# Kernel optimization log

Measured on AMD Instinct MI355X. Metric: run time of the kernel, lower is better.

The kernel has to match this reference:

```python
import jax, jax.numpy as jnp
import numpy as np

B, T, C, H = 4, 4096, 1024, 64

def setup_inputs() -> dict:
    key = jax.random.key(0)
    kx, kq, kk, kv = jax.random.split(key, 4)
    # nn.Linear weights are [out, in]; we store them that way and use einsum.
    s = 1.0 / np.sqrt(C)
    return {
        "x": jax.random.normal(kx, (B, T, C), dtype=jnp.float32),
        "Wq": jax.random.uniform(kq, (H, C), dtype=jnp.float32, minval=-s, maxval=s),
        "Wk": jax.random.uniform(kk, (H, C), dtype=jnp.float32, minval=-s, maxval=s),
        "Wv": jax.random.uniform(kv, (H, C), dtype=jnp.float32, minval=-s, maxval=s),
    }

def reference(x, Wq, Wk, Wv):
    # x: [B, T, C]; W*: [H, C] (torch Linear layout)
    Q = jnp.einsum('btc,hc->bth', x, Wq)  # [B, T, H]
    K = jnp.einsum('btc,hc->bth', x, Wk)
    V = jnp.einsum('btc,hc->bth', x, Wv)
    scale = K.shape[-1] ** -0.5
    scores = jnp.einsum('bqh,bkh->bqk', Q, K) * scale  # [B, T, T]
    Tn = x.shape[1]
    causal = jnp.tril(jnp.ones((Tn, Tn), dtype=bool))
    scores = jnp.where(causal, scores, -jnp.inf)
    attn = jax.nn.softmax(scores, axis=-1)
    return jnp.einsum('bqk,bkh->bqh', attn, V)  # [B, T, H]
```

## Files before the change

kernel.cpp:

```cpp
#include <hip/hip_runtime.h>
#include <hip/hip_bf16.h>

#define B_ 4
#define T_ 4096
#define C_ 1024
#define H_ 64

typedef __bf16 bf16x8 __attribute__((ext_vector_type(8)));
typedef float f32x4 __attribute__((ext_vector_type(4)));
typedef unsigned short u16x8 __attribute__((ext_vector_type(8)));

union Frag8 { uint4 u; bf16x8 b; u16x8 s; };

__device__ inline unsigned short bfbits(float f) {
  union { __hip_bfloat16 h; unsigned short u; } cv;
  cv.h = __float2bfloat16(f);
  return cv.u;
}

__device__ inline float b2f(unsigned u) {
  union { unsigned i; float f; } c; c.i = u << 16; return c.f;
}

__device__ inline bf16x8 ldb8(const unsigned short* p) {
  Frag8 f; f.u = *(const uint4*)p; return f.b;
}

__device__ inline bf16x8 asbf(uint4 u) { Frag8 f; f.u = u; return f.b; }

__device__ inline unsigned pkbf(float a, float b) {
  union { float f; unsigned u; } ua, ub; ua.f = a; ub.f = b;
  return __builtin_amdgcn_perm(ub.u + 0x8000u, ua.u + 0x8000u, 0x07060302u);
}

__device__ inline Frag8 packA(float4 a0, float4 a1) {
  Frag8 af;
  af.s[0] = bfbits(a0.x); af.s[1] = bfbits(a0.y);
  af.s[2] = bfbits(a0.z); af.s[3] = bfbits(a0.w);
  af.s[4] = bfbits(a1.x); af.s[5] = bfbits(a1.y);
  af.s[6] = bfbits(a1.z); af.s[7] = bfbits(a1.w);
  return af;
}

__device__ inline void gload16(const void* g, void* l) {
  __builtin_amdgcn_global_load_lds(
      (const __attribute__((address_space(1))) unsigned int*)g,
      (__attribute__((address_space(3))) unsigned int*)l, 16, 0, 0);
}

__global__ __launch_bounds__(256) void wconv(const float* __restrict__ Wq,
                                             const float* __restrict__ Wk,
                                             const float* __restrict__ Wv,
                                             unsigned short* __restrict__ Wb) {
  int i = blockIdx.x * 256 + threadIdx.x;
  size_t e = (size_t)i * 4;
  const float* src = (e < 65536) ? (Wq + e)
                   : (e < 131072 ? (Wk + (e - 65536)) : (Wv + (e - 131072)));
  float4 v = *(const float4*)src;
  unsigned long long o =
      (unsigned long long)bfbits(v.x)
    | ((unsigned long long)bfbits(v.y) << 16)
    | ((unsigned long long)bfbits(v.z) << 32)
    | ((unsigned long long)bfbits(v.w) << 48);
  *(unsigned long long*)(Wb + e) = o;
}

__global__ __launch_bounds__(256) void qkv_proj(const float* __restrict__ x,
                                                const unsigned short* __restrict__ Wb,
                                                unsigned short* __restrict__ qkv,
                                                unsigned short* __restrict__ Vt) {
  __shared__ float xs[2][2048];
  __shared__ unsigned short Wsh[2][12288];
  const int lane = threadIdx.x & 63;
  const int wave = threadIdx.x >> 6;
  const int q16 = lane & 15, quad = lane >> 4;
  const int x7 = q16 & 7;
  const size_t row0 = (size_t)blockIdx.x * 32;

  const int sr = lane >> 4;
  const int sc_pos = lane & 15;
  const int rloc = lane >> 3;
  const int cpos = lane & 7;

  f32x4 acc[2][3] = {};

  auto stage = [&](int buf, int kc) {
#pragma unroll
    for (int ii = 0; ii < 2; ++ii) {
      int i = wave * 2 + ii;
      int r = i * 4 + sr;
      int sg = (sc_pos >> 1) ^ (r & 7);
      const float* gp = x + (row0 + r) * C_ + kc + sg * 8 + (sc_pos & 1) * 4;
      gload16(gp, &xs[buf][i * 256]);
    }
#pragma unroll
    for (int jj = 0; jj < 6; ++jj) {
      int j = wave * 6 + jj;
      int g = j * 8 + rloc;
      const unsigned short* gp = Wb + (size_t)(g >> 6) * 65536
                                    + (size_t)(g & 63) * C_ + kc + (cpos ^ rloc) * 8;
      gload16(gp, &Wsh[buf][j * 512]);
    }
  };

  stage(0, 0);
  __syncthreads();

  int cur = 0;
  for (int t = 0; t < 16; ++t) {
    if (t < 15) stage(cur ^ 1, (t + 1) * 64);
    const float* Xc = xs[cur];
    const unsigned short* Wc = Wsh[cur];
#pragma unroll
    for (int s = 0; s < 2; ++s) {
      bf16x8 bf[3];
#pragma unroll
      for (int ct = 0; ct < 3; ++ct) {
        int g = wave * 48 + ct * 16 + q16;
        bf[ct] = ldb8(&Wc[g * 64 + (((s * 4 + quad) ^ x7) * 8)]);
      }
#pragma unroll
      for (int rt = 0; rt < 2; ++rt) {
        int r = rt * 16 + q16;
        int p = ((s * 4 + quad) ^ (r & 7)) * 8;
        const float* ap = &Xc[r * 64 + p];
        float4 a0 = *(const float4*)ap;
        float4 a1 = *(const float4*)(ap + 4);
        Frag8 af = packA(a0, a1);
#pragma unroll
        for (int ct = 0; ct < 3; ++ct)
          acc[rt][ct] = __builtin_amdgcn_mfma_f32_16x16x32_bf16(
              af.b, bf[ct], acc[rt][ct], 0, 0, 0);
      }
    }
    __syncthreads();
    cur ^= 1;
  }

  const int bb = (int)(blockIdx.x >> 7);
#pragma unroll
  for (int rt = 0; rt < 2; ++rt) {
    const int t0 = (int)(row0 - (size_t)bb * T_) + rt * 16 + quad * 4;
#pragma unroll
    for (int ct = 0; ct < 3; ++ct) {
      int gcol = wave * 48 + ct * 16;
      int mat = gcol >> 6, h = (gcol & 63) + q16;
      if (mat == 2) {
        ushort4 v;
        v.x = bfbits(acc[rt][ct][0]); v.y = bfbits(acc[rt][ct][1]);
        v.z = bfbits(acc[rt][ct][2]); v.w = bfbits(acc[rt][ct][3]);
        *(ushort4*)(Vt + ((size_t)bb * H_ + h) * T_ + t0) = v;
      } else {
        float scale = (mat == 0) ? 0.18033688f : 1.0f;
#pragma unroll
        for (int r = 0; r < 4; ++r) {
          size_t row = row0 + rt * 16 + quad * 4 + r;
          qkv[(size_t)mat * 1048576 + row * H_ + h] = bfbits(acc[rt][ct][r] * scale);
        }
      }
    }
  }
}

__global__ __launch_bounds__(256) void attn(const unsigned short* __restrict__ Q,
                                            const unsigned short* __restrict__ K,
                                            const unsigned short* __restrict__ Vt,
                                            float* __restrict__ part,
                                            int lgch, int nslots) {
  const int b = blockIdx.x >> 6;
  const int qblk = 63 - (blockIdx.x & 63);
  const int ki = qblk + 1;
  const int c = blockIdx.y;
  const int cst = c << lgch;
  if (cst >= ki) return;
  const int tcnt = 1 << lgch;
  const int kend = (ki < cst + tcnt) ? ki : cst + tcnt;

  __shared__ unsigned short Ks[2][4096];
  __shared__ unsigned short Vs[2][4096];
  const int lane = threadIdx.x & 63;
  const int wave = threadIdx.x >> 6;
  const int q16 = lane & 15, quad = lane >> 4;
  const int x7 = q16 & 7;
  const int rloc = lane >> 3, cpos = lane & 7;

  const unsigned short* Qb = Q + (size_t)b * T_ * H_;
  const unsigned short* Kb = K + (size_t)b * T_ * H_;
  const unsigned short* Vtb = Vt + (size_t)b * H_ * T_;

  auto stage = [&](int buf, int kt) {
    const int kkb = kt * 64;
#pragma unroll
    for (int ii = 0; ii < 2; ++ii) {
      int i = wave * 2 + ii;
      gload16(Kb + (size_t)(kkb + i * 8 + rloc) * H_ + (cpos ^ rloc) * 8,
              &Ks[buf][i * 512]);
      gload16(Vtb + (size_t)(i * 8 + rloc) * T_ + kkb + (cpos ^ rloc) * 8,
              &Vs[buf][i * 512]);
    }
  };

  const int q0w = qblk * 64 + wave * 16;
  bf16x8 qf0 = ldb8(Qb + (size_t)(q0w + q16) * H_ + quad * 8);
  bf16x8 qf1 = ldb8(Qb + (size_t)(q0w + q16) * H_ + 32 + quad * 8);

  f32x4 o0 = {0.f, 0.f, 0.f, 0.f}, o1 = o0, o2 = o0, o3 = o0;
  float m = -3.0e38f, l = 0.0f;
  const int q_abs = q0w + q16;
  const int src0 = q16 + 32 * (quad & 1);
  const int kbsel = quad >> 1;

  stage(0, cst);
  __syncthreads();

  int cur = 0;
  for (int kt = cst; kt < kend; ++kt) {
    const int kkb = kt * 64;
    if (kt + 1 < kend) stage(cur ^ 1, kt + 1);
    const unsigned short* Kc = Ks[cur];
    const unsigned short* Vc = Vs[cur];

    f32x4 st[4];
#pragma unroll
    for (int kb = 0; kb < 4; ++kb) {
      bf16x8 ka0 = ldb8(&Kc[(kb * 16 + q16) * 64 + ((quad ^ x7) * 8)]);
      bf16x8 ka1 = ldb8(&Kc[(kb * 16 + q16) * 64 + (((quad + 4) ^ x7) * 8)]);
      f32x4 s = {0.f, 0.f, 0.f, 0.f};
      s = __builtin_amdgcn_mfma_f32_16x16x32_bf16(ka0, qf0, s, 0, 0, 0);
      s = __builtin_amdgcn_mfma_f32_16x16x32_bf16(ka1, qf1, s, 0, 0, 0);
      st[kb] = s;
    }
    if (kt == ki - 1) {
#pragma unroll
      for (int kb = 0; kb < 4; ++kb)
#pragma unroll
        for (int r = 0; r < 4; ++r)
          if (kkb + kb * 16 + quad * 4 + r > q_abs) st[kb][r] = -3.0e38f;
    }

    float mloc = fmaxf(fmaxf(st[0][0], st[0][1]), fmaxf(st[0][2], st[0][3]));
#pragma unroll
    for (int kb = 1; kb < 4; ++kb)
      mloc = fmaxf(mloc, fmaxf(fmaxf(st[kb][0], st[kb][1]), fmaxf(st[kb][2], st[kb][3])));
    mloc = fmaxf(mloc, __shfl_xor(mloc, 16));
    mloc = fmaxf(mloc, __shfl_xor(mloc, 32));
    const bool defer = __all(mloc - m <= 8.0f);
    const float mnew = defer ? m : fmaxf(m, mloc);
    float lsum = 0.f;
    unsigned pk[4][2];
#pragma unroll
    for (int kb = 0; kb < 4; ++kb) {
      float p0 = exp2f(st[kb][0] - mnew);
      float p1 = exp2f(st[kb][1] - mnew);
      float p2 = exp2f(st[kb][2] - mnew);
      float p3 = exp2f(st[kb][3] - mnew);
      lsum += (p0 + p1) + (p2 + p3);
      pk[kb][0] = pkbf(p0, p1);
      pk[kb][1] = pkbf(p2, p3);
    }
    lsum += __shfl_xor(lsum, 16);
    lsum += __shfl_xor(lsum, 32);
    if (defer) {
      l += lsum;
    } else {
      float alpha = exp2f(m - mnew);
      l = l * alpha + lsum;
      m = mnew;
      float ar0 = __shfl(alpha, quad * 4 + 0);
      float ar1 = __shfl(alpha, quad * 4 + 1);
      float ar2 = __shfl(alpha, quad * 4 + 2);
      float ar3 = __shfl(alpha, quad * 4 + 3);
      o0[0] *= ar0; o0[1] *= ar1; o0[2] *= ar2; o0[3] *= ar3;
      o1[0] *= ar0; o1[1] *= ar1; o1[2] *= ar2; o1[3] *= ar3;
      o2[0] *= ar0; o2[1] *= ar1; o2[2] *= ar2; o2[3] *= ar3;
      o3[0] *= ar0; o3[1] *= ar1; o3[2] *= ar2; o3[3] *= ar3;
    }

#pragma unroll
    for (int kb2 = 0; kb2 < 2; ++kb2) {
      int xA = __shfl((int)pk[2 * kb2][0], src0);
      int xB = __shfl((int)pk[2 * kb2 + 1][0], src0);
      int yA = __shfl((int)pk[2 * kb2][1], src0);
      int yB = __shfl((int)pk[2 * kb2 + 1][1], src0);
      int zA = __shfl((int)pk[2 * kb2][0], src0 + 16);
      int zB = __shfl((int)pk[2 * kb2 + 1][0], src0 + 16);
      int wA = __shfl((int)pk[2 * kb2][1], src0 + 16);
      int wB = __shfl((int)pk[2 * kb2 + 1][1], src0 + 16);
      Frag8 pf;
      pf.u.x = (unsigned)(kbsel ? xB : xA);
      pf.u.y = (unsigned)(kbsel ? yB : yA);
      pf.u.z = (unsigned)(kbsel ? zB : zA);
      pf.u.w = (unsigned)(kbsel ? wB : wA);
      int vp = ((kb2 * 4 + quad) ^ x7) * 8;
      bf16x8 v0 = ldb8(&Vc[(q16 + 0)  * 64 + vp]);
      bf16x8 v1 = ldb8(&Vc[(q16 + 16) * 64 + vp]);
      bf16x8 v2 = ldb8(&Vc[(q16 + 32) * 64 + vp]);
      bf16x8 v3 = ldb8(&Vc[(q16 + 48) * 64 + vp]);
      o0 = __builtin_amdgcn_mfma_f32_16x16x32_bf16(pf.b, v0, o0, 0, 0, 0);
      o1 = __builtin_amdgcn_mfma_f32_16x16x32_bf16(pf.b, v1, o1, 0, 0, 0);
      o2 = __builtin_amdgcn_mfma_f32_16x16x32_bf16(pf.b, v2, o2, 0, 0, 0);
      o3 = __builtin_amdgcn_mfma_f32_16x16x32_bf16(pf.b, v3, o3, 0, 0, 0);
    }
    __syncthreads();
    cur ^= 1;
  }

  const int qtl = qblk * 4 + wave;
  float* Pf = part + ((size_t)((b << 8) + qtl) * nslots + c) * 544;
  unsigned* Pw = (unsigned*)Pf;
  Pw[0 * 64 + lane] = pkbf(o0[0], o0[1]);
  Pw[1 * 64 + lane] = pkbf(o0[2], o0[3]);
  Pw[2 * 64 + lane] = pkbf(o1[0], o1[1]);
  Pw[3 * 64 + lane] = pkbf(o1[2], o1[3]);
  Pw[4 * 64 + lane] = pkbf(o2[0], o2[1]);
  Pw[5 * 64 + lane] = pkbf(o2[2], o2[3]);
  Pw[6 * 64 + lane] = pkbf(o3[0], o3[1]);
  Pw[7 * 64 + lane] = pkbf(o3[2], o3[3]);
  if (quad == 0) { Pf[512 + q16] = m; Pf[528 + q16] = l; }
}

__global__ __launch_bounds__(256) void attn_merge(const float* __restrict__ part,
                                                  float* __restrict__ out,
                                                  int lgch, int nslots) {
  const int qt = blockIdx.x;
  const int qtl = qt & 255, b = qt >> 8;
  const int ki = (qtl >> 2) + 1;
  const int nch = (ki + (1 << lgch) - 1) >> lgch;
  const int t = threadIdx.x;
  const int row = t >> 4, col0 = (t & 15) * 4;
  const int i = (col0 >> 4) * 4 + (row & 3);
  const int lane0 = (row >> 2) * 16 + (col0 & 15);
  const int sh = 16 * (i & 1);
  const float* P0 = part + (size_t)qt * nslots * 544;
  float M = -3.0e38f;
  for (int c2 = 0; c2 < nch; ++c2) M = fmaxf(M, P0[c2 * 544 + 512 + row]);
  float L = 0.f;
  float ax = 0.f, ay = 0.f, az = 0.f, aw = 0.f;
  for (int c2 = 0; c2 < nch; ++c2) {
    const float* P = P0 + c2 * 544;
    float w = exp2f(P[512 + row] - M);
    L += w * P[528 + row];
    const unsigned* Pw = (const unsigned*)P;
    uint4 wd = *(const uint4*)&Pw[(i >> 1) * 64 + lane0];
    ax += w * b2f((wd.x >> sh) & 0xffffu);
    ay += w * b2f((wd.y >> sh) & 0xffffu);
    az += w * b2f((wd.z >> sh) & 0xffffu);
    aw += w * b2f((wd.w >> sh) & 0xffffu);
  }
  float inv = 1.0f / L;
  float4 r = {ax * inv, ay * inv, az * inv, aw * inv};
  *(float4*)(out + ((size_t)b * T_ + qtl * 16 + row) * H_ + col0) = r;
}

extern "C" void kernel_launch(void* const* d_in, const int* in_sizes, int n_in,
                              void* d_out, int out_size, void* d_ws, size_t ws_size,
                              hipStream_t stream) {
  const float* x  = (const float*)d_in[0];
  const float* Wq = (const float*)d_in[1];
  const float* Wk = (const float*)d_in[2];
  const float* Wv = (const float*)d_in[3];
  float* out = (float*)d_out;
  unsigned short* ws = (unsigned short*)d_ws;

  unsigned short* Wb  = ws;
  unsigned short* qkv = ws + 196608;
  unsigned short* Vt  = qkv + (size_t)2 * 1048576;
  float* part = (float*)(ws + 196608 + (size_t)3 * 1048576);

  const size_t base_bytes = ((size_t)196608 + (size_t)3 * 1048576) * 2;
  const size_t need16 = base_bytes + (size_t)1024 * 16 * 544 * 4;
  int lgch = 3, ny = 8, nslots = 8;
  if (ws_size >= need16) { lgch = 2; ny = 16; nslots = 16; }

  wconv<<<192, 256, 0, stream>>>(Wq, Wk, Wv, Wb);
  qkv_proj<<<512, 256, 0, stream>>>(x, Wb, qkv, Vt);
  attn<<<dim3(256, ny), 256, 0, stream>>>(qkv, qkv + 1048576, Vt, part, lgch, nslots);
  attn_merge<<<1024, 256, 0, stream>>>(part, out, lgch, nslots);
}
```

Before: 162.7 us.

## Process two 16-row query tiles per wave to double K/V tile reuse

Each attention block now covers 128 query rows instead of 64, with each wave holding two 16-row query fragments that share every staged K/V tile in LDS. This halves global K/V traffic and staging work per query, and halves the grid. The per-row lsum reduction is moved out of the loop to a single shuffle at the end. Risks include higher register pressure from doubled accumulators, less causal load balance at coarser granularity, and fewer blocks to fill the GPU.

After: 185.9 us. +14.2%, slower.

```diff
diff --git a/kernel.cpp b/kernel.cpp
--- a/kernel.cpp
+++ b/kernel.cpp
@@ -25,8 +25,6 @@
 __device__ inline bf16x8 ldb8(const unsigned short* p) {
   Frag8 f; f.u = *(const uint4*)p; return f.b;
 }
-
-__device__ inline bf16x8 asbf(uint4 u) { Frag8 f; f.u = u; return f.b; }
 
 __device__ inline unsigned pkbf(float a, float b) {
   union { float f; unsigned u; } ua, ub; ua.f = a; ub.f = b;
@@ -167,14 +165,14 @@
                                             const unsigned short* __restrict__ Vt,
                                             float* __restrict__ part,
                                             int lgch, int nslots) {
-  const int b = blockIdx.x >> 6;
-  const int qblk = 63 - (blockIdx.x & 63);
-  const int ki = qblk + 1;
+  const int b = blockIdx.x >> 5;
+  const int qblk = 31 - (blockIdx.x & 31);
+  const int ki_block = 2 * qblk + 2;
   const int c = blockIdx.y;
   const int cst = c << lgch;
-  if (cst >= ki) return;
+  if (cst >= ki_block) return;
   const int tcnt = 1 << lgch;
-  const int kend = (ki < cst + tcnt) ? ki : cst + tcnt;
+  const int kend = (ki_block < cst + tcnt) ? ki_block : cst + tcnt;
 
   __shared__ unsigned short Ks[2][4096];
   __shared__ unsigned short Vs[2][4096];
@@ -200,13 +198,19 @@
     }
   };
 
-  const int q0w = qblk * 64 + wave * 16;
-  bf16x8 qf0 = ldb8(Qb + (size_t)(q0w + q16) * H_ + quad * 8);
-  bf16x8 qf1 = ldb8(Qb + (size_t)(q0w + q16) * H_ + 32 + quad * 8);
-
-  f32x4 o0 = {0.f, 0.f, 0.f, 0.f}, o1 = o0, o2 = o0, o3 = o0;
-  float m = -3.0e38f, l = 0.0f;
-  const int q_abs = q0w + q16;
+  const int q0w = qblk * 128 + wave * 32;
+  int f0[2];  f0[0] = q0w;             f0[1] = q0w + 16;
+  int kiF[2]; kiF[0] = (f0[0] >> 6) + 1; kiF[1] = (f0[1] >> 6) + 1;
+
+  bf16x8 qf[2][2];
+#pragma unroll
+  for (int rt = 0; rt < 2; ++rt) {
+    qf[rt][0] = ldb8(Qb + (size_t)(f0[rt] + q16) * H_ + quad * 8);
+    qf[rt][1] = ldb8(Qb + (size_t)(f0[rt] + q16) * H_ + 32 + quad * 8);
+  }
+
+  f32x4 o[2][4] = {};
+  float m[2] = {-3.0e38f, -3.0e38f}, l[2] = {0.0f, 0.0f};
   const int src0 = q16 + 32 * (quad & 1);
   const int kbsel = quad >> 1;
 
@@ -220,103 +224,131 @@
     const unsigned short* Kc = Ks[cur];
     const unsigned short* Vc = Vs[cur];
 
-    f32x4 st[4];
+    f32x4 st[2][4];
 #pragma unroll
     for (int kb = 0; kb < 4; ++kb) {
       bf16x8 ka0 = ldb8(&Kc[(kb * 16 + q16) * 64 + ((quad ^ x7) * 8)]);
       bf16x8 ka1 = ldb8(&Kc[(kb * 16 + q16) * 64 + (((quad + 4) ^ x7) * 8)]);
-      f32x4 s = {0.f, 0.f, 0.f, 0.f};
-      s = __builtin_amdgcn_mfma_f32_16x16x32_bf16(ka0, qf0, s, 0, 0, 0);
-      s = __builtin_amdgcn_mfma_f32_16x16x32_bf16(ka1, qf1, s, 0, 0, 0);
-      st[kb] = s;
-    }
-    if (kt == ki - 1) {
-#pragma unroll
-      for (int kb = 0; kb < 4; ++kb)
-#pragma unroll
-        for (int r = 0; r < 4; ++r)
-          if (kkb + kb * 16 + quad * 4 + r > q_abs) st[kb][r] = -3.0e38f;
-    }
-
-    float mloc = fmaxf(fmaxf(st[0][0], st[0][1]), fmaxf(st[0][2], st[0][3]));
-#pragma unroll
-    for (int kb = 1; kb < 4; ++kb)
-      mloc = fmaxf(mloc, fmaxf(fmaxf(st[kb][0], st[kb][1]), fmaxf(st[kb][2], st[kb][3])));
-    mloc = fmaxf(mloc, __shfl_xor(mloc, 16));
-    mloc = fmaxf(mloc, __shfl_xor(mloc, 32));
-    const bool defer = __all(mloc - m <= 8.0f);
-    const float mnew = defer ? m : fmaxf(m, mloc);
-    float lsum = 0.f;
-    unsigned pk[4][2];
-#pragma unroll
-    for (int kb = 0; kb < 4; ++kb) {
-      float p0 = exp2f(st[kb][0] - mnew);
-      float p1 = exp2f(st[kb][1] - mnew);
-      float p2 = exp2f(st[kb][2] - mnew);
-      float p3 = exp2f(st[kb][3] - mnew);
-      lsum += (p0 + p1) + (p2 + p3);
-      pk[kb][0] = pkbf(p0, p1);
-      pk[kb][1] = pkbf(p2, p3);
-    }
-    lsum += __shfl_xor(lsum, 16);
-    lsum += __shfl_xor(lsum, 32);
-    if (defer) {
-      l += lsum;
-    } else {
-      float alpha = exp2f(m - mnew);
-      l = l * alpha + lsum;
-      m = mnew;
-      float ar0 = __shfl(alpha, quad * 4 + 0);
-      float ar1 = __shfl(alpha, quad * 4 + 1);
-      float ar2 = __shfl(alpha, quad * 4 + 2);
-      float ar3 = __shfl(alpha, quad * 4 + 3);
-      o0[0] *= ar0; o0[1] *= ar1; o0[2] *= ar2; o0[3] *= ar3;
-      o1[0] *= ar0; o1[1] *= ar1; o1[2] *= ar2; o1[3] *= ar3;
-      o2[0] *= ar0; o2[1] *= ar1; o2[2] *= ar2; o2[3] *= ar3;
-      o3[0] *= ar0; o3[1] *= ar1; o3[2] *= ar2; o3[3] *= ar3;
+#pragma unroll
+      for (int rt = 0; rt < 2; ++rt) {
+        if (kt < kiF[rt]) {
+          f32x4 s = {0.f, 0.f, 0.f, 0.f};
+          s = __builtin_amdgcn_mfma_f32_16x16x32_bf16(ka0, qf[rt][0], s, 0, 0, 0);
+          s = __builtin_amdgcn_mfma_f32_16x16x32_bf16(ka1, qf[rt][1], s, 0, 0, 0);
+          st[rt][kb] = s;
+        }
+      }
+    }
+#pragma unroll
+    for (int rt = 0; rt < 2; ++rt) {
+      if (kt == kiF[rt] - 1) {
+        const int qa = f0[rt] + q16;
+#pragma unroll
+        for (int kb = 0; kb < 4; ++kb)
+#pragma unroll
+          for (int r = 0; r < 4; ++r)
+            if (kkb + kb * 16 + quad * 4 + r > qa) st[rt][kb][r] = -3.0e38f;
+      }
+    }
+
+    unsigned pk[2][4][2];
+#pragma unroll
+    for (int rt = 0; rt < 2; ++rt) {
+      if (kt < kiF[rt]) {
+        float mloc = fmaxf(fmaxf(st[rt][0][0], st[rt][0][1]),
+                           fmaxf(st[rt][0][2], st[rt][0][3]));
+#pragma unroll
+        for (int kb = 1; kb < 4; ++kb)
+          mloc = fmaxf(mloc, fmaxf(fmaxf(st[rt][kb][0], st[rt][kb][1]),
+                                   fmaxf(st[rt][kb][2], st[rt][kb][3])));
+        mloc = fmaxf(mloc, __shfl_xor(mloc, 16));
+        mloc = fmaxf(mloc, __shfl_xor(mloc, 32));
+        const bool defer = __all(mloc - m[rt] <= 8.0f);
+        const float mnew = defer ? m[rt] : fmaxf(m[rt], mloc);
+        float lsum = 0.f;
+#pragma unroll
+        for (int kb = 0; kb < 4; ++kb) {
+          float p0 = exp2f(st[rt][kb][0] - mnew);
+          float p1 = exp2f(st[rt][kb][1] - mnew);
+          float p2 = exp2f(st[rt][kb][2] - mnew);
+          float p3 = exp2f(st[rt][kb][3] - mnew);
+          lsum += (p0 + p1) + (p2 + p3);
+          pk[rt][kb][0] = pkbf(p0, p1);
+          pk[rt][kb][1] = pkbf(p2, p3);
+        }
+        if (defer) {
+          l[rt] += lsum;
+        } else {
+          float alpha = exp2f(m[rt] - mnew);
+          l[rt] = l[rt] * alpha + lsum;
+          m[rt] = mnew;
+          float ar0 = __shfl(alpha, quad * 4 + 0);
+          float ar1 = __shfl(alpha, quad * 4 + 1);
+          float ar2 = __shfl(alpha, quad * 4 + 2);
+          float ar3 = __shfl(alpha, quad * 4 + 3);
+#pragma unroll
+          for (int ct = 0; ct < 4; ++ct) {
+            o[rt][ct][0] *= ar0; o[rt][ct][1] *= ar1;
+            o[rt][ct][2] *= ar2; o[rt][ct][3] *= ar3;
+          }
+        }
+      }
     }
 
 #pragma unroll
     for (int kb2 = 0; kb2 < 2; ++kb2) {
-      int xA = __shfl((int)pk[2 * kb2][0], src0);
-      int xB = __shfl((int)pk[2 * kb2 + 1][0], src0);
-      int yA = __shfl((int)pk[2 * kb2][1], src0);
-      int yB = __shfl((int)pk[2 * kb2 + 1][1], src0);
-      int zA = __shfl((int)pk[2 * kb2][0], src0 + 16);
-      int zB = __shfl((int)pk[2 * kb2 + 1][0], src0 + 16);
-      int wA = __shfl((int)pk[2 * kb2][1], src0 + 16);
-      int wB = __shfl((int)pk[2 * kb2 + 1][1], src0 + 16);
-      Frag8 pf;
-      pf.u.x = (unsigned)(kbsel ? xB : xA);
-      pf.u.y = (unsigned)(kbsel ? yB : yA);
-      pf.u.z = (unsigned)(kbsel ? zB : zA);
-      pf.u.w = (unsigned)(kbsel ? wB : wA);
       int vp = ((kb2 * 4 + quad) ^ x7) * 8;
       bf16x8 v0 = ldb8(&Vc[(q16 + 0)  * 64 + vp]);
       bf16x8 v1 = ldb8(&Vc[(q16 + 16) * 64 + vp]);
       bf16x8 v2 = ldb8(&Vc[(q16 + 32) * 64 + vp]);
       bf16x8 v3 = ldb8(&Vc[(q16 + 48) * 64 + vp]);
-      o0 = __builtin_amdgcn_mfma_f32_16x16x32_bf16(pf.b, v0, o0, 0, 0, 0);
-      o1 = __builtin_amdgcn_mfma_f32_16x16x32_bf16(pf.b, v1, o1, 0, 0, 0);
-      o2 = __builtin_amdgcn_mfma_f32_16x16x32_bf16(pf.b, v2, o2, 0, 0, 0);
-      o3 = __builtin_amdgcn_mfma_f32_16x16x32_bf16(pf.b, v3, o3, 0, 0, 0);
+#pragma unroll
+      for (int rt = 0; rt < 2; ++rt) {
+        if (kt < kiF[rt]) {
+          int xA = __shfl((int)pk[rt][2 * kb2][0], src0);
+          int xB = __shfl((int)pk[rt][2 * kb2 + 1][0], src0);
+          int yA = __shfl((int)pk[rt][2 * kb2][1], src0);
+          int yB = __shfl((int)pk[rt][2 * kb2 + 1][1], src0);
+          int zA = __shfl((int)pk[rt][2 * kb2][0], src0 + 16);
+          int zB = __shfl((int)pk[rt][2 * kb2 + 1][0], src0 + 16);
+          int wA = __shfl((int)pk[rt][2 * kb2][1], src0 + 16);
+          int wB = __shfl((int)pk[rt][2 * kb2 + 1][1], src0 + 16);
+          Frag8 pf;
+          pf.u.x = (unsigned)(kbsel ? xB : xA);
+          pf.u.y = (unsigned)(kbsel ? yB : yA);
+          pf.u.z = (unsigned)(kbsel ? zB : zA);
+          pf.u.w = (unsigned)(kbsel ? wB : wA);
+          o[rt][0] = __builtin_amdgcn_mfma_f32_16x16x32_bf16(pf.b, v0, o[rt][0], 0, 0, 0);
+          o[rt][1] = __builtin_amdgcn_mfma_f32_16x16x32_bf16(pf.b, v1, o[rt][1], 0, 0, 0);
+          o[rt][2] = __builtin_amdgcn_mfma_f32_16x16x32_bf16(pf.b, v2, o[rt][2], 0, 0, 0);
+          o[rt][3] = __builtin_amdgcn_mfma_f32_16x16x32_bf16(pf.b, v3, o[rt][3], 0, 0, 0);
+        }
+      }
     }
     __syncthreads();
     cur ^= 1;
   }
 
-  const int qtl = qblk * 4 + wave;
-  float* Pf = part + ((size_t)((b << 8) + qtl) * nslots + c) * 544;
-  unsigned* Pw = (unsigned*)Pf;
-  Pw[0 * 64 + lane] = pkbf(o0[0], o0[1]);
-  Pw[1 * 64 + lane] = pkbf(o0[2], o0[3]);
-  Pw[2 * 64 + lane] = pkbf(o1[0], o1[1]);
-  Pw[3 * 64 + lane] = pkbf(o1[2], o1[3]);
-  Pw[4 * 64 + lane] = pkbf(o2[0], o2[1]);
-  Pw[5 * 64 + lane] = pkbf(o2[2], o2[3]);
-  Pw[6 * 64 + lane] = pkbf(o3[0], o3[1]);
-  Pw[7 * 64 + lane] = pkbf(o3[2], o3[3]);
-  if (quad == 0) { Pf[512 + q16] = m; Pf[528 + q16] = l; }
+#pragma unroll
+  for (int rt = 0; rt < 2; ++rt) {
+    if ((cst << 6) <= f0[rt]) {
+      const int qtl = f0[rt] >> 4;
+      float lr = l[rt];
+      lr += __shfl_xor(lr, 16);
+      lr += __shfl_xor(lr, 32);
+      float* Pf = part + ((size_t)((b << 8) + qtl) * nslots + c) * 544;
+      unsigned* Pw = (unsigned*)Pf;
+      Pw[0 * 64 + lane] = pkbf(o[rt][0][0], o[rt][0][1]);
+      Pw[1 * 64 + lane] = pkbf(o[rt][0][2], o[rt][0][3]);
+      Pw[2 * 64 + lane] = pkbf(o[rt][1][0], o[rt][1][1]);
+      Pw[3 * 64 + lane] = pkbf(o[rt][1][2], o[rt][1][3]);
+      Pw[4 * 64 + lane] = pkbf(o[rt][2][0], o[rt][2][1]);
+      Pw[5 * 64 + lane] = pkbf(o[rt][2][2], o[rt][2][3]);
+      Pw[6 * 64 + lane] = pkbf(o[rt][3][0], o[rt][3][1]);
+      Pw[7 * 64 + lane] = pkbf(o[rt][3][2], o[rt][3][3]);
+      if (quad == 0) { Pf[512 + q16] = m[rt]; Pf[528 + q16] = lr; }
+    }
+  }
 }
 
 __global__ __launch_bounds__(256) void attn_merge(const float* __restrict__ part,
@@ -374,6 +406,6 @@
 
   wconv<<<192, 256, 0, stream>>>(Wq, Wk, Wv, Wb);
   qkv_proj<<<512, 256, 0, stream>>>(x, Wb, qkv, Vt);
-  attn<<<dim3(256, ny), 256, 0, stream>>>(qkv, qkv + 1048576, Vt, part, lgch, nslots);
+  attn<<<dim3(128, ny), 256, 0, stream>>>(qkv, qkv + 1048576, Vt, part, lgch, nslots);
   attn_merge<<<1024, 256, 0, stream>>>(part, out, lgch, nslots);
 }
```

## Permute K rows and swap MFMA operands to drop P-fragment shuffles

Applied to the files above, without the earlier changes.

Loads K tiles into LDS with a permuted row order so the score MFMA output layout matches the P operand layout needed for the PV MFMA. This removes the eight cross-lane shuffles per step that built P fragments, and the per-row alpha shuffles, because the PV MFMA now has V as the A operand and output rows align with lanes. The row-sum reduction moves out of the loop to the end, and partial outputs are stored as contiguous uint2 words, with the merge kernel's reads changed to match. It depends on the permuted mask offsets and the new output layout staying consistent.

Result: no change. 161.8 us (-0.5%).

```diff
diff --git a/kernel.cpp b/kernel.cpp
--- a/kernel.cpp
+++ b/kernel.cpp
@@ -25,8 +25,6 @@
 __device__ inline bf16x8 ldb8(const unsigned short* p) {
   Frag8 f; f.u = *(const uint4*)p; return f.b;
 }
-
-__device__ inline bf16x8 asbf(uint4 u) { Frag8 f; f.u = u; return f.b; }
 
 __device__ inline unsigned pkbf(float a, float b) {
   union { float f; unsigned u; } ua, ub; ua.f = a; ub.f = b;
@@ -188,12 +186,19 @@
   const unsigned short* Kb = K + (size_t)b * T_ * H_;
   const unsigned short* Vtb = Vt + (size_t)b * H_ * T_;
 
+  int psi_[2];
+#pragma unroll
+  for (int ii = 0; ii < 2; ++ii) {
+    int g = (wave * 2 + ii) * 8 + rloc;
+    psi_[ii] = 8 * ((g & 15) >> 2) + (g & 3) + 4 * ((g >> 4) & 1) + 32 * (g >> 5);
+  }
+
   auto stage = [&](int buf, int kt) {
     const int kkb = kt * 64;
 #pragma unroll
     for (int ii = 0; ii < 2; ++ii) {
       int i = wave * 2 + ii;
-      gload16(Kb + (size_t)(kkb + i * 8 + rloc) * H_ + (cpos ^ rloc) * 8,
+      gload16(Kb + (size_t)(kkb + psi_[ii]) * H_ + (cpos ^ rloc) * 8,
               &Ks[buf][i * 512]);
       gload16(Vtb + (size_t)(i * 8 + rloc) * T_ + kkb + (cpos ^ rloc) * 8,
               &Vs[buf][i * 512]);
@@ -204,11 +209,9 @@
   bf16x8 qf0 = ldb8(Qb + (size_t)(q0w + q16) * H_ + quad * 8);
   bf16x8 qf1 = ldb8(Qb + (size_t)(q0w + q16) * H_ + 32 + quad * 8);
 
-  f32x4 o0 = {0.f, 0.f, 0.f, 0.f}, o1 = o0, o2 = o0, o3 = o0;
+  f32x4 o[4] = {};
   float m = -3.0e38f, l = 0.0f;
   const int q_abs = q0w + q16;
-  const int src0 = q16 + 32 * (quad & 1);
-  const int kbsel = quad >> 1;
 
   stage(0, cst);
   __syncthreads();
@@ -231,11 +234,14 @@
       st[kb] = s;
     }
     if (kt == ki - 1) {
-#pragma unroll
-      for (int kb = 0; kb < 4; ++kb)
+      const int kb8q = kkb + 8 * quad;
+#pragma unroll
+      for (int kb = 0; kb < 4; ++kb) {
+        const int kof = kb8q + 4 * (kb & 1) + 32 * (kb >> 1);
 #pragma unroll
         for (int r = 0; r < 4; ++r)
-          if (kkb + kb * 16 + quad * 4 + r > q_abs) st[kb][r] = -3.0e38f;
+          if (kof + r > q_abs) st[kb][r] = -3.0e38f;
+      }
     }
 
     float mloc = fmaxf(fmaxf(st[0][0], st[0][1]), fmaxf(st[0][2], st[0][3]));
@@ -258,65 +264,54 @@
       pk[kb][0] = pkbf(p0, p1);
       pk[kb][1] = pkbf(p2, p3);
     }
-    lsum += __shfl_xor(lsum, 16);
-    lsum += __shfl_xor(lsum, 32);
     if (defer) {
       l += lsum;
     } else {
       float alpha = exp2f(m - mnew);
       l = l * alpha + lsum;
       m = mnew;
-      float ar0 = __shfl(alpha, quad * 4 + 0);
-      float ar1 = __shfl(alpha, quad * 4 + 1);
-      float ar2 = __shfl(alpha, quad * 4 + 2);
-      float ar3 = __shfl(alpha, quad * 4 + 3);
-      o0[0] *= ar0; o0[1] *= ar1; o0[2] *= ar2; o0[3] *= ar3;
-      o1[0] *= ar0; o1[1] *= ar1; o1[2] *= ar2; o1[3] *= ar3;
-      o2[0] *= ar0; o2[1] *= ar1; o2[2] *= ar2; o2[3] *= ar3;
-      o3[0] *= ar0; o3[1] *= ar1; o3[2] *= ar2; o3[3] *= ar3;
-    }
-
-#pragma unroll
-    for (int kb2 = 0; kb2 < 2; ++kb2) {
-      int xA = __shfl((int)pk[2 * kb2][0], src0);
-      int xB = __shfl((int)pk[2 * kb2 + 1][0], src0);
-      int yA = __shfl((int)pk[2 * kb2][1], src0);
-      int yB = __shfl((int)pk[2 * kb2 + 1][1], src0);
-      int zA = __shfl((int)pk[2 * kb2][0], src0 + 16);
-      int zB = __shfl((int)pk[2 * kb2 + 1][0], src0 + 16);
-      int wA = __shfl((int)pk[2 * kb2][1], src0 + 16);
-      int wB = __shfl((int)pk[2 * kb2 + 1][1], src0 + 16);
+#pragma unroll
+      for (int ct = 0; ct < 4; ++ct) {
+        o[ct][0] *= alpha; o[ct][1] *= alpha;
+        o[ct][2] *= alpha; o[ct][3] *= alpha;
+      }
+    }
+
+#pragma unroll
+    for (int ks = 0; ks < 2; ++ks) {
       Frag8 pf;
-      pf.u.x = (unsigned)(kbsel ? xB : xA);
-      pf.u.y = (unsigned)(kbsel ? yB : yA);
-      pf.u.z = (unsigned)(kbsel ? zB : zA);
-      pf.u.w = (unsigned)(kbsel ? wB : wA);
-      int vp = ((kb2 * 4 + quad) ^ x7) * 8;
+      pf.u.x = pk[2 * ks][0];
+      pf.u.y = pk[2 * ks][1];
+      pf.u.z = pk[2 * ks + 1][0];
+      pf.u.w = pk[2 * ks + 1][1];
+      int vp = ((ks * 4 + quad) ^ x7) * 8;
       bf16x8 v0 = ldb8(&Vc[(q16 + 0)  * 64 + vp]);
       bf16x8 v1 = ldb8(&Vc[(q16 + 16) * 64 + vp]);
       bf16x8 v2 = ldb8(&Vc[(q16 + 32) * 64 + vp]);
       bf16x8 v3 = ldb8(&Vc[(q16 + 48) * 64 + vp]);
-      o0 = __builtin_amdgcn_mfma_f32_16x16x32_bf16(pf.b, v0, o0, 0, 0, 0);
-      o1 = __builtin_amdgcn_mfma_f32_16x16x32_bf16(pf.b, v1, o1, 0, 0, 0);
-      o2 = __builtin_amdgcn_mfma_f32_16x16x32_bf16(pf.b, v2, o2, 0, 0, 0);
-      o3 = __builtin_amdgcn_mfma_f32_16x16x32_bf16(pf.b, v3, o3, 0, 0, 0);
+      o[0] = __builtin_amdgcn_mfma_f32_16x16x32_bf16(v0, pf.b, o[0], 0, 0, 0);
+      o[1] = __builtin_amdgcn_mfma_f32_16x16x32_bf16(v1, pf.b, o[1], 0, 0, 0);
+      o[2] = __builtin_amdgcn_mfma_f32_16x16x32_bf16(v2, pf.b, o[2], 0, 0, 0);
+      o[3] = __builtin_amdgcn_mfma_f32_16x16x32_bf16(v3, pf.b, o[3], 0, 0, 0);
     }
     __syncthreads();
     cur ^= 1;
   }
 
   const int qtl = qblk * 4 + wave;
+  float lr = l;
+  lr += __shfl_xor(lr, 16);
+  lr += __shfl_xor(lr, 32);
   float* Pf = part + ((size_t)((b << 8) + qtl) * nslots + c) * 544;
   unsigned* Pw = (unsigned*)Pf;
-  Pw[0 * 64 + lane] = pkbf(o0[0], o0[1]);
-  Pw[1 * 64 + lane] = pkbf(o0[2], o0[3]);
-  Pw[2 * 64 + lane] = pkbf(o1[0], o1[1]);
-  Pw[3 * 64 + lane] = pkbf(o1[2], o1[3]);
-  Pw[4 * 64 + lane] = pkbf(o2[0], o2[1]);
-  Pw[5 * 64 + lane] = pkbf(o2[2], o2[3]);
-  Pw[6 * 64 + lane] = pkbf(o3[0], o3[1]);
-  Pw[7 * 64 + lane] = pkbf(o3[2], o3[3]);
-  if (quad == 0) { Pf[512 + q16] = m; Pf[528 + q16] = l; }
+#pragma unroll
+  for (int ct = 0; ct < 4; ++ct) {
+    uint2 w;
+    w.x = pkbf(o[ct][0], o[ct][1]);
+    w.y = pkbf(o[ct][2], o[ct][3]);
+    *(uint2*)&Pw[(ct * 64 + lane) * 2] = w;
+  }
+  if (quad == 0) { Pf[512 + q16] = m; Pf[528 + q16] = lr; }
 }
 
 __global__ __launch_bounds__(256) void attn_merge(const float* __restrict__ part,
@@ -327,10 +322,11 @@
   const int ki = (qtl >> 2) + 1;
   const int nch = (ki + (1 << lgch) - 1) >> lgch;
   const int t = threadIdx.x;
-  const int row = t >> 4, col0 = (t & 15) * 4;
-  const int i = (col0 >> 4) * 4 + (row & 3);
-  const int lane0 = (row >> 2) * 16 + (col0 & 15);
-  const int sh = 16 * (i & 1);
+  const int row = t >> 4;
+  const int col0 = (t & 15) * 4;
+  const int ct = col0 >> 4;
+  const int quad_s = (col0 >> 2) & 3;
+  const int lane0 = quad_s * 16 + row;
   const float* P0 = part + (size_t)qt * nslots * 544;
   float M = -3.0e38f;
   for (int c2 = 0; c2 < nch; ++c2) M = fmaxf(M, P0[c2 * 544 + 512 + row]);
@@ -338,14 +334,14 @@
   float ax = 0.f, ay = 0.f, az = 0.f, aw = 0.f;
   for (int c2 = 0; c2 < nch; ++c2) {
     const float* P = P0 + c2 * 544;
-    float w = exp2f(P[512 + row] - M);
-    L += w * P[528 + row];
-    const unsigned* Pw = (const unsigned*)P;
-    uint4 wd = *(const uint4*)&Pw[(i >> 1) * 64 + lane0];
-    ax += w * b2f((wd.x >> sh) & 0xffffu);
-    ay += w * b2f((wd.y >> sh) & 0xffffu);
-    az += w * b2f((wd.z >> sh) & 0xffffu);
-    aw += w * b2f((wd.w >> sh) & 0xffffu);
+    float wgt = exp2f(P[512 + row] - M);
+    L += wgt * P[528 + row];
+    const unsigned* Pww = (const unsigned*)P;
+    uint2 wd = *(const uint2*)&Pww[(ct * 64 + lane0) * 2];
+    ax += wgt * b2f(wd.x & 0xffffu);
+    ay += wgt * b2f(wd.x >> 16);
+    az += wgt * b2f(wd.y & 0xffffu);
+    aw += wgt * b2f(wd.y >> 16);
   }
   float inv = 1.0f / L;
   float4 r = {ax * inv, ay * inv, az * inv, aw * inv};
```
